# Kernel optimization log

Measured on AMD Instinct MI355X. Metric: run time of the kernel, lower is better.

## Reference

```python
import jax, jax.numpy as jnp
import numpy as np
from jax import lax

N_CLASS, SOS, EOS, NEG = 5, 0, 4, -10000.0


def _lstm_dir(x, Wih, Whh, bih, bhh, reverse):
    # x: (T, B, Din); PyTorch gate order i, f, g, o
    T, B, _ = x.shape
    Hd = Whh.shape[1]
    h0 = jnp.zeros((B, Hd), x.dtype)

    def step(carry, xt):
        h, c = carry
        g = xt @ Wih.T + h @ Whh.T + bih + bhh
        i, f, gg, o = jnp.split(g, 4, axis=-1)
        c = jax.nn.sigmoid(f) * c + jax.nn.sigmoid(i) * jnp.tanh(gg)
        h = jax.nn.sigmoid(o) * jnp.tanh(c)
        return (h, c), h

    xs = x[::-1] if reverse else x
    _, hs = lax.scan(step, (h0, h0), xs)
    return hs[::-1] if reverse else hs


def _forward(input_ids, tags, mask, emb, convs, lstm_params, lin_w, lin_b, transition):
    T, B = mask.shape
    x = emb[input_ids][:, None]  # (N, 1, L, E)
    pooled = []
    for w, b in convs:  # w: (K, 1, size, E)
        c = lax.conv_general_dilated(x, w, (1, 1), 'VALID',
                                     dimension_numbers=('NCHW', 'OIHW', 'NCHW'))
        c = jax.nn.relu(c[..., 0] + b[None, :, None])  # (N, K, L-size+1)
        pooled.append(jnp.max(c, axis=2))              # max-pool over length
    para = jnp.concatenate(pooled, axis=1)             # (N, 3K)
    h = para.reshape(B, T, -1).transpose(1, 0, 2)      # (T, B, 3K); equal para_len
    for (Wf, Uf, bf, cf, Wb, Ub, bb, cb) in lstm_params:  # 2-layer BiLSTM (eval: no dropout)
        hf = _lstm_dir(h, Wf, Uf, bf, cf, False)
        hb = _lstm_dir(h, Wb, Ub, bb, cb, True)
        h = jnp.concatenate([hf, hb], axis=-1)
    m = mask[..., None]
    feats = ((h * m) @ lin_w.T + lin_b) * m            # (T, B, 5)

    # CRF forward algorithm (log partition)
    alpha0 = jnp.full((B, N_CLASS), NEG, feats.dtype).at[:, SOS].set(0.0)

    def step(alpha, inp):
        feat, mt = inp
        s = alpha[:, None, :] + transition[None] + feat[:, :, None]
        new = jax.nn.logsumexp(s, axis=-1)
        return new * mt[:, None] + alpha * (1.0 - mt[:, None]), None

    alpha, _ = lax.scan(step, alpha0, (feats, mask))
    fwd_score = jax.nn.logsumexp(alpha + transition[EOS][None], axis=-1)

    # gold path score
    tags_ext = jnp.concatenate([jnp.full((1, B), SOS, tags.dtype), tags], 0)  # (T+1, B)
    emit = jnp.take_along_axis(feats, tags[..., None], axis=-1)[..., 0]       # (T, B)
    trans = transition[tags_ext[1:], tags_ext[:-1]]                           # (T, B)
    gold = jnp.sum((emit + trans) * mask, axis=0)
    lengths = mask.sum(0).astype(jnp.int32)
    last = tags_ext[lengths, jnp.arange(B)]
    gold = gold + transition[EOS, last]
    return (fwd_score - gold).sum()


def setup_inputs() -> dict:
    key = jax.random.key(0)
    ks = jax.random.split(key, 32)
    B, T, L, V, E, K, H = 8, 64, 64, 50000, 768, 256, 64
    N = B * T
    inp = {}
    inp['input_ids'] = jax.random.randint(ks[0], (N, L), 1, V)
    inp['tags'] = jax.random.randint(ks[1], (T, B), 1, 4)  # B/I/O tags
    inp['mask'] = jnp.ones((T, B), jnp.float32)
    inp['para_len'] = jnp.full((B,), T, jnp.int32)
    inp['emb'] = jax.random.normal(ks[2], (V, E)) * 0.1
    for i, sz in enumerate((3, 4, 5)):
        inp[f'cw{sz}'] = jax.random.normal(ks[3 + i], (K, 1, sz, E)) * (1.0 / np.sqrt(sz * E))
        inp[f'cb{sz}'] = jnp.zeros((K,), jnp.float32)
    kidx = 6
    for layer, din in ((0, 3 * K), (1, 2 * H)):
        for d in 'fb':
            inp[f'Wih{layer}{d}'] = jax.random.normal(ks[kidx], (4 * H, din)) * (1.0 / np.sqrt(din)); kidx += 1
            inp[f'Whh{layer}{d}'] = jax.random.normal(ks[kidx], (4 * H, H)) * (1.0 / np.sqrt(H)); kidx += 1
            inp[f'bih{layer}{d}'] = jnp.zeros((4 * H,), jnp.float32)
            inp[f'bhh{layer}{d}'] = jnp.zeros((4 * H,), jnp.float32)
    inp['lin_w'] = jax.random.normal(ks[kidx], (N_CLASS, 2 * H)) * 0.1; kidx += 1
    inp['lin_b'] = jnp.zeros((N_CLASS,), jnp.float32)
    tr = jax.random.normal(ks[kidx], (N_CLASS, N_CLASS))
    inp['transition'] = tr.at[SOS, :].set(NEG).at[:, EOS].set(NEG)
    return inp


def reference(input_ids, tags, mask, para_len, emb, cw3, cb3, cw4, cb4, cw5, cb5,
              Wih0f, Whh0f, bih0f, bhh0f, Wih0b, Whh0b, bih0b, bhh0b,
              Wih1f, Whh1f, bih1f, bhh1f, Wih1b, Whh1b, bih1b, bhh1b,
              lin_w, lin_b, transition):
    convs = ((cw3, cb3), (cw4, cb4), (cw5, cb5))
    lstm_params = ((Wih0f, Whh0f, bih0f, bhh0f, Wih0b, Whh0b, bih0b, bhh0b),
                   (Wih1f, Whh1f, bih1f, bhh1f, Wih1b, Whh1b, bih1b, bhh1b))
    return _forward(input_ids, tags, mask, emb, convs, lstm_params, lin_w, lin_b, transition)
```

## Files before the change

### kernel.cpp

```cpp
#include <hip/hip_runtime.h>
#include <cstdint>
#include <cstddef>

#define DEV __device__ __forceinline__

typedef __bf16 bf16x8 __attribute__((ext_vector_type(8)));
typedef float f32x4 __attribute__((ext_vector_type(4)));

#define NEG_VAL -10000.0f

DEV unsigned int f2bf(float f) {
    unsigned int u = __float_as_uint(f);
    return (u + 0x7FFFu + ((u >> 16) & 1u)) >> 16;
}
DEV unsigned int pk2(float a, float b) { return f2bf(a) | (f2bf(b) << 16); }

DEV float sigf(float x)  { return __builtin_amdgcn_rcpf(1.f + __expf(-x)); }
DEV float tanhff(float x){ return 2.f * __builtin_amdgcn_rcpf(1.f + __expf(-2.f * x)) - 1.f; }

__global__ void cast_all_kernel(const float* __restrict__ cw3,
                                const float* __restrict__ cw4,
                                const float* __restrict__ cw5,
                                const float* __restrict__ Wih0f,
                                const float* __restrict__ Wih0b,
                                const float* __restrict__ Wih1f,
                                const float* __restrict__ Wih1b,
                                unsigned short* __restrict__ wbc,
                                unsigned short* __restrict__ wih0c,
                                unsigned short* __restrict__ wih1c) {
    int tid = blockIdx.x * blockDim.x + threadIdx.x;
    const float* src;
    uint4* dstp;
    if (tid < 294912) {
        int g   = tid & 3;
        int col = (tid >> 2) & 255;
        int c   = (tid >> 10) % 24;
        int p   = tid / (24 * 256 * 4);
        int sz, j; const float* W;
        if (p < 3)      { sz = 3; j = p;     W = cw3; }
        else if (p < 7) { sz = 4; j = p - 3; W = cw4; }
        else            { sz = 5; j = p - 7; W = cw5; }
        src = W + ((size_t)col * sz + j) * 768 + c * 32 + g * 8;
        dstp = reinterpret_cast<uint4*>(wbc) +
               ((size_t)(p * 24 + c) * 1024 + (col >> 4) * 64 + g * 16 + (col & 15));
    } else if (tid < 294912 + 49152) {
        int u   = tid - 294912;
        int g   = u & 3;
        int col = (u >> 2) & 255;
        int kc  = (u >> 10) % 24;
        int dir = u / (24 * 256 * 4);
        const float* W = dir ? Wih0b : Wih0f;
        src = W + (size_t)col * 768 + kc * 32 + g * 8;
        dstp = reinterpret_cast<uint4*>(wih0c) +
               ((size_t)(dir * 24 + kc) * 1024 + (col >> 4) * 64 + g * 16 + (col & 15));
    } else if (tid < 294912 + 49152 + 8192) {
        int u   = tid - 294912 - 49152;
        int g   = u & 3;
        int col = (u >> 2) & 255;
        int kc  = (u >> 10) % 4;
        int dir = u / (4 * 256 * 4);
        const float* W = dir ? Wih1b : Wih1f;
        src = W + (size_t)col * 128 + kc * 32 + g * 8;
        dstp = reinterpret_cast<uint4*>(wih1c) +
               ((size_t)(dir * 4 + kc) * 1024 + (col >> 4) * 64 + g * 16 + (col & 15));
    } else return;
    float4 a = *(const float4*)(src);
    float4 b = *(const float4*)(src + 4);
    *dstp = make_uint4(pk2(a.x, a.y), pk2(a.z, a.w), pk2(b.x, b.y), pk2(b.z, b.w));
}

template<int SZ>
DEV void conv_body(const int* __restrict__ ids,
                   const float* __restrict__ emb,
                   const unsigned short* __restrict__ wbc,
                   const float* __restrict__ cb,
                   unsigned short* __restrict__ para_bf,
                   int pair, int szi, int pbase,
                   unsigned short* Xlds)
{
    int tid  = threadIdx.x;
    int lane = tid & 63;
    int nw   = tid >> 6;
    int l15  = lane & 15;
    int q    = lane >> 4;
    int n0   = pair * 2;

    int srow  = tid >> 1;
    int shalf = tid & 1;
    int sid   = ids[(n0 + (srow >> 6)) * 64 + (srow & 63)];
    const float* embrow = emb + (size_t)sid * 768 + shalf * 16;
    int skey = (srow >> 1) & 3;
    int xo0 = srow * 32 + (((2 * shalf)     ^ skey) * 8);
    int xo1 = srow * 32 + (((2 * shalf + 1) ^ skey) * 8);

    int vlaneB = nw * 2048 + lane * 8;

    f32x4 acc[8][4];
    #pragma unroll
    for (int a = 0; a < 8; a++)
        #pragma unroll
        for (int t = 0; t < 4; t++) acc[a][t] = (f32x4){0.f, 0.f, 0.f, 0.f};

    bf16x8 bfr[2][4];
    float4 e0, e1, e2, e3;

    {
        e0 = ((const float4*)embrow)[0];
        e1 = ((const float4*)embrow)[1];
        e2 = ((const float4*)embrow)[2];
        e3 = ((const float4*)embrow)[3];
        const unsigned short* bt = wbc + (size_t)(pbase * 24) * 8192 + vlaneB;
        #pragma unroll
        for (int t = 0; t < 4; t++)
            bfr[0][t] = *(const bf16x8*)(bt + t * 512);
        uint4 p0 = make_uint4(pk2(e0.x, e0.y), pk2(e0.z, e0.w),
                              pk2(e1.x, e1.y), pk2(e1.z, e1.w));
        uint4 p1 = make_uint4(pk2(e2.x, e2.y), pk2(e2.z, e2.w),
                              pk2(e3.x, e3.y), pk2(e3.z, e3.w));
        *(uint4*)&Xlds[xo0] = p0;
        *(uint4*)&Xlds[xo1] = p1;
        asm volatile("s_waitcnt lgkmcnt(0)" ::: "memory");
        __builtin_amdgcn_s_barrier();
    }

    int cbase = pbase * 24;
    for (int c2 = 0; c2 < 24; c2 += 2, cbase += 2) {
        #pragma unroll
        for (int s2 = 0; s2 < 2 * SZ; ++s2) {
            const int half = (s2 < SZ) ? 0 : 1;
            const int j    = s2 - half * SZ;
            const int par  = s2 & 1;
            {
                const int sP = s2 + 1;
                const int offP = (sP < SZ) ? sP * 24
                               : (sP < 2 * SZ ? (sP - SZ) * 24 + 1 : 2);
                const unsigned short* bt =
                    wbc + (size_t)(cbase + offP) * 8192 + vlaneB;
                #pragma unroll
                for (int t = 0; t < 4; t++)
                    bfr[par ^ 1][t] = *(const bf16x8*)(bt + t * 512);
            }
            if (s2 == 0 || s2 == SZ) {
                int cE = half ? c2 + 2 : c2 + 1; if (cE > 23) cE = 0;
                const float* sp = embrow + cE * 32;
                e0 = ((const float4*)sp)[0];
                e1 = ((const float4*)sp)[1];
                e2 = ((const float4*)sp)[2];
                e3 = ((const float4*)sp)[3];
            }

            const unsigned short* Xb = Xlds + half * 4096;
            {
                bf16x8 af[4];
                #pragma unroll
                for (int a = 0; a < 4; a++) {
                    int pp = 16 * a + l15 + j; if (pp > 63) pp = 63;
                    af[a] = *(const bf16x8*)(
                        &Xb[pp * 32 + ((q ^ ((pp >> 1) & 3)) * 8)]);
                }
                __builtin_amdgcn_s_setprio(1);
                #pragma unroll
                for (int a = 0; a < 4; a++)
                    #pragma unroll
                    for (int t = 0; t < 4; t++)
                        acc[a][t] = __builtin_amdgcn_mfma_f32_16x16x32_bf16(
                            af[a], bfr[par][t], acc[a][t], 0, 0, 0);
                __builtin_amdgcn_s_setprio(0);
            }
            {
                bf16x8 af[4];
                #pragma unroll
                for (int a = 0; a < 4; a++) {
                    int pp = 16 * a + l15 + j; if (pp > 63) pp = 63;
                    int xr = 64 + pp;
                    af[a] = *(const bf16x8*)(
                        &Xb[xr * 32 + ((q ^ ((xr >> 1) & 3)) * 8)]);
                }
                __builtin_amdgcn_s_setprio(1);
                #pragma unroll
                for (int a = 0; a < 4; a++)
                    #pragma unroll
                    for (int t = 0; t < 4; t++)
                        acc[4 + a][t] = __builtin_amdgcn_mfma_f32_16x16x32_bf16(
                            af[a], bfr[par][t], acc[4 + a][t], 0, 0, 0);
                __builtin_amdgcn_s_setprio(0);
            }

            if (j == SZ - 1) {
                unsigned short* Xw = Xlds + (half ^ 1) * 4096;
                uint4 p0 = make_uint4(pk2(e0.x, e0.y), pk2(e0.z, e0.w),
                                      pk2(e1.x, e1.y), pk2(e1.z, e1.w));
                uint4 p1 = make_uint4(pk2(e2.x, e2.y), pk2(e2.z, e2.w),
                                      pk2(e3.x, e3.y), pk2(e3.z, e3.w));
                *(uint4*)&Xw[xo0] = p0;
                *(uint4*)&Xw[xo1] = p1;
                asm volatile("s_waitcnt lgkmcnt(0)" ::: "memory");
                __builtin_amdgcn_s_barrier();
            }
        }
    }

    int pmax = 64 - SZ;
    #pragma unroll
    for (int t = 0; t < 4; t++) {
        int colb = nw * 64 + t * 16;
        float bias = cb[colb + l15];
        #pragma unroll
        for (int s = 0; s < 2; s++) {
            float m = 0.0f;
            #pragma unroll
            for (int a4 = 0; a4 < 4; a4++) {
                #pragma unroll
                for (int r = 0; r < 4; r++) {
                    int p = 16 * a4 + q * 4 + r;
                    float v = acc[s * 4 + a4][t][r] + bias;
                    v = v > 0.f ? v : 0.f;
                    if (p <= pmax) m = v > m ? v : m;
                }
            }
            m = fmaxf(m, __shfl_xor(m, 16));
            m = fmaxf(m, __shfl_xor(m, 32));
            if (lane < 16) {
                int n = n0 + s;
                int row = (n & 63) * 8 + (n >> 6);
                para_bf[(size_t)row * 768 + szi * 256 + colb + lane] =
                    (unsigned short)f2bf(m);
            }
        }
    }
}

__global__ __launch_bounds__(256, 2) void conv_pool_kernel(
    const int* __restrict__ ids,
    const float* __restrict__ emb,
    const unsigned short* __restrict__ wbc,
    const float* __restrict__ cb3, const float* __restrict__ cb4,
    const float* __restrict__ cb5,
    unsigned short* __restrict__ para_bf)
{
    __shared__ unsigned short Xlds[2][4096];
    int bx   = blockIdx.x;
    int szi  = 2 - (bx >> 8);
    int pair = bx & 255;
    if (szi == 0)
        conv_body<3>(ids, emb, wbc, cb3, para_bf, pair, 0, 0, &Xlds[0][0]);
    else if (szi == 1)
        conv_body<4>(ids, emb, wbc, cb4, para_bf, pair, 1, 3, &Xlds[0][0]);
    else
        conv_body<5>(ids, emb, wbc, cb5, para_bf, pair, 2, 7, &Xlds[0][0]);
}

template<int KC>
__global__ __launch_bounds__(256) void gemm_in_kernel(
    const unsigned short* __restrict__ xbf,
    const unsigned short* __restrict__ wihc,
    const float* __restrict__ bihF, const float* __restrict__ bhhF,
    const float* __restrict__ bihB, const float* __restrict__ bhhB,
    float* __restrict__ gates)
{
    const int din = KC * 32;
    int bx   = blockIdx.x;
    int dir  = bx >> 4;
    int rowg = (bx >> 1) & 7;
    int colg = bx & 1;
    int tid  = threadIdx.x;
    int lane = tid & 63;
    int wid  = tid >> 6;
    int mw   = wid >> 1;
    int nw   = wid & 1;
    int l15  = lane & 15;
    int q    = lane >> 4;

    const float* bih = dir ? bihB : bihF;
    const float* bhh = dir ? bhhB : bhhF;
    const unsigned short* wt = wihc + (size_t)dir * KC * 8192;

    const unsigned short* arow[2];
    #pragma unroll
    for (int a = 0; a < 2; a++)
        arow[a] = xbf + (size_t)(rowg * 64 + mw * 32 + a * 16 + l15) * din + q * 8;
    const unsigned short* bbase = wt + (colg * 8 + nw * 4) * 512 + lane * 8;

    f32x4 acc[2][4];
    #pragma unroll
    for (int a = 0; a < 2; a++)
        #pragma unroll
        for (int t = 0; t < 4; t++) acc[a][t] = (f32x4){0.f, 0.f, 0.f, 0.f};

    bf16x8 afb[3][2], bfb[3][4];
    #pragma unroll
    for (int s = 0; s < 3; s++) {
        int k0 = (s < KC) ? s : KC - 1;
        if (s < 2) {
            #pragma unroll
            for (int a = 0; a < 2; a++)
                afb[s][a] = *(const bf16x8*)(arow[a] + k0 * 32);
            #pragma unroll
            for (int t = 0; t < 4; t++)
                bfb[s][t] = *(const bf16x8*)(bbase + (size_t)k0 * 8192 + t * 512);
        }
    }

    #pragma unroll 3
    for (int kc = 0; kc < KC; ++kc) {
        const int p = kc % 3;
        int kn = (kc + 2 < KC) ? kc + 2 : KC - 1;
        const int pn = (kc + 2) % 3;
        #pragma unroll
        for (int a = 0; a < 2; a++)
            afb[pn][a] = *(const bf16x8*)(arow[a] + kn * 32);
        #pragma unroll
        for (int t = 0; t < 4; t++)
            bfb[pn][t] = *(const bf16x8*)(bbase + (size_t)kn * 8192 + t * 512);
        #pragma unroll
        for (int a = 0; a < 2; a++)
            #pragma unroll
            for (int t = 0; t < 4; t++)
                acc[a][t] = __builtin_amdgcn_mfma_f32_16x16x32_bf16(
                    afb[p][a], bfb[p][t], acc[a][t], 0, 0, 0);
    }

    #pragma unroll
    for (int t = 0; t < 4; t++) {
        int nn = colg * 128 + nw * 64 + t * 16 + l15;
        float bb = bih[nn] + bhh[nn];
        float* gp = gates + ((size_t)dir * 256 + nn) * 512 +
                    rowg * 64 + mw * 32 + q * 4;
        #pragma unroll
        for (int a = 0; a < 2; a++) {
            f32x4 v = acc[a][t];
            v[0] += bb; v[1] += bb; v[2] += bb; v[3] += bb;
            *(f32x4*)(gp + a * 16) = v;
        }
    }
}

__global__ __launch_bounds__(256) void lstm_rec_kernel(
    const float* __restrict__ gates,
    const float* __restrict__ WhhF, const float* __restrict__ WhhB,
    float* __restrict__ houtF,
    unsigned short* __restrict__ houtB)
{
    int dir = blockIdx.x;
    const float* Whh = dir ? WhhB : WhhF;
    const float* gin = gates + (size_t)dir * 256 * 512;

    __shared__ unsigned short h16[2][16 * 64];

    int tid  = threadIdx.x;
    int lane = tid & 63;
    int w    = tid >> 6;
    int l15  = lane & 15;
    int q    = lane >> 4;
    int hh   = 16 * w + l15;

    bf16x8 Bf[4][2];
    #pragma unroll
    for (int g = 0; g < 4; g++)
        #pragma unroll
        for (int kh = 0; kh < 2; kh++) {
            const float* wp = Whh + (size_t)(g * 64 + hh) * 64 + kh * 32 + q * 8;
            float4 f0 = *(const float4*)wp;
            float4 f1 = *(const float4*)(wp + 4);
            bf16x8 r;
            r[0] = (__bf16)f0.x; r[1] = (__bf16)f0.y;
            r[2] = (__bf16)f0.z; r[3] = (__bf16)f0.w;
            r[4] = (__bf16)f1.x; r[5] = (__bf16)f1.y;
            r[6] = (__bf16)f1.z; r[7] = (__bf16)f1.w;
            Bf[g][kh] = r;
        }

    const float* pg[4];
    #pragma unroll
    for (int g = 0; g < 4; g++)
        pg[g] = gin + ((size_t)(g * 64 + hh)) * 512 + 4 * q;

    for (int i = tid; i < 2 * 16 * 64; i += 256)
        ((unsigned short*)h16)[i] = 0;
    float cst[4] = {0.f, 0.f, 0.f, 0.f};
    __syncthreads();

    int t0 = dir ? 63 : 0;
    f32x4 gv[4];
    #pragma unroll
    for (int g = 0; g < 4; g++) gv[g] = *(const f32x4*)(pg[g] + t0 * 8);

    for (int s = 0; s < 64; ++s) {
        int t = dir ? 63 - s : s;
        const unsigned short* hb = h16[s & 1];
        int slot0 = q ^ (l15 & 7);
        int slot1 = (4 + q) ^ (l15 & 7);
        bf16x8 a0 = *(const bf16x8*)&hb[l15 * 64 + slot0 * 8];
        bf16x8 a1 = *(const bf16x8*)&hb[l15 * 64 + slot1 * 8];

        f32x4 acc[4];
        #pragma unroll
        for (int g = 0; g < 4; g++) {
            acc[g] = __builtin_amdgcn_mfma_f32_16x16x32_bf16(a0, Bf[g][0], gv[g], 0, 0, 0);
            acc[g] = __builtin_amdgcn_mfma_f32_16x16x32_bf16(a1, Bf[g][1], acc[g], 0, 0, 0);
        }

        int sn = (s + 1 < 64) ? s + 1 : 63;
        int t2 = dir ? 63 - sn : sn;
        f32x4 n0 = *(const f32x4*)(pg[0] + t2 * 8);
        f32x4 n1 = *(const f32x4*)(pg[1] + t2 * 8);
        f32x4 n2 = *(const f32x4*)(pg[2] + t2 * 8);
        f32x4 n3 = *(const f32x4*)(pg[3] + t2 * 8);

        if (q < 2) {
            unsigned short* hw = h16[(s + 1) & 1];
            #pragma unroll
            for (int r = 0; r < 4; r++) {
                int b = 4 * q + r;
                float gi = acc[0][r];
                float gf = acc[1][r];
                float gg = acc[2][r];
                float go = acc[3][r];
                float cn = sigf(gf) * cst[r] + sigf(gi) * tanhff(gg);
                float hv = sigf(go) * tanhff(cn);
                cst[r] = cn;
                int slot = (hh >> 3) ^ (b & 7);
                hw[b * 64 + slot * 8 + (hh & 7)] = (unsigned short)f2bf(hv);
                size_t oi = ((size_t)t * 8 + b) * 128 + dir * 64 + hh;
                if (houtF) houtF[oi] = hv;
                houtB[oi] = (unsigned short)f2bf(hv);
            }
        }
        __syncthreads();
        gv[0] = n0; gv[1] = n1; gv[2] = n2; gv[3] = n3;
    }
}

__global__ __launch_bounds__(512) void crf_kernel(
    const float* __restrict__ h1,
    const float* __restrict__ lin_w,
    const float* __restrict__ lin_b,
    const float* __restrict__ mask,
    const int* __restrict__ tags,
    const float* __restrict__ trans,
    float* __restrict__ out) {
    __shared__ float feats[64][8][5];
    __shared__ float wl[5][128];
    __shared__ float msk[512];
    __shared__ int   tgs[512];
    __shared__ float fwd_s[8], gold_s[8];
    __shared__ float tr[25], trE[5], lb[5];
    int tid = threadIdx.x;
    if (tid < 25) tr[tid] = trans[tid];
    if (tid < 5) { trE[tid] = trans[20 + tid]; lb[tid] = lin_b[tid]; }
    msk[tid] = mask[tid];
    tgs[tid] = tags[tid];
    if (tid < 128) {
        #pragma unroll
        for (int i = 0; i < 5; i++) wl[i][tid] = lin_w[i * 128 + tid];
    }
    __syncthreads();

    {
        const float4* h4 = (const float4*)(h1 + (size_t)tid * 128);
        float a0 = 0.f, a1 = 0.f, a2 = 0.f, a3 = 0.f, a4 = 0.f;
        for (int e4 = 0; e4 < 32; e4++) {
            float4 hv = h4[e4];
            int e = e4 * 4;
            a0 += hv.x * wl[0][e] + hv.y * wl[0][e+1] + hv.z * wl[0][e+2] + hv.w * wl[0][e+3];
            a1 += hv.x * wl[1][e] + hv.y * wl[1][e+1] + hv.z * wl[1][e+2] + hv.w * wl[1][e+3];
            a2 += hv.x * wl[2][e] + hv.y * wl[2][e+1] + hv.z * wl[2][e+2] + hv.w * wl[2][e+3];
            a3 += hv.x * wl[3][e] + hv.y * wl[3][e+1] + hv.z * wl[3][e+2] + hv.w * wl[3][e+3];
            a4 += hv.x * wl[4][e] + hv.y * wl[4][e+1] + hv.z * wl[4][e+2] + hv.w * wl[4][e+3];
        }
        float m = msk[tid];
        int t = tid >> 3, b = tid & 7;
        feats[t][b][0] = (m * a0 + lb[0]) * m;
        feats[t][b][1] = (m * a1 + lb[1]) * m;
        feats[t][b][2] = (m * a2 + lb[2]) * m;
        feats[t][b][3] = (m * a3 + lb[3]) * m;
        feats[t][b][4] = (m * a4 + lb[4]) * m;
    }
    __syncthreads();

    if (tid < 40) {
        int b = tid / 5, i = tid % 5;
        float alpha = (i == 0) ? 0.f : NEG_VAL;
        float trow[5];
        #pragma unroll
        for (int j2 = 0; j2 < 5; j2++) trow[j2] = tr[i * 5 + j2];
        for (int t = 0; t < 64; t++) {
            float s0, s1, s2, s3, s4;
            s0 = __shfl(alpha, b * 5 + 0, 64) + trow[0];
            s1 = __shfl(alpha, b * 5 + 1, 64) + trow[1];
            s2 = __shfl(alpha, b * 5 + 2, 64) + trow[2];
            s3 = __shfl(alpha, b * 5 + 3, 64) + trow[3];
            s4 = __shfl(alpha, b * 5 + 4, 64) + trow[4];
            float mx = fmaxf(fmaxf(fmaxf(s0, s1), fmaxf(s2, s3)), s4);
            float sum = expf(s0 - mx) + expf(s1 - mx) + expf(s2 - mx) +
                        expf(s3 - mx) + expf(s4 - mx);
            float lse = mx + logf(sum) + feats[t][b][i];
            float mt = msk[t * 8 + b];
            alpha = mt * lse + (1.f - mt) * alpha;
        }
        float v = alpha + trE[i];
        float m0 = __shfl(v, b * 5 + 0, 64);
        float m1 = __shfl(v, b * 5 + 1, 64);
        float m2 = __shfl(v, b * 5 + 2, 64);
        float m3 = __shfl(v, b * 5 + 3, 64);
        float m4 = __shfl(v, b * 5 + 4, 64);
        float mx = fmaxf(fmaxf(fmaxf(m0, m1), fmaxf(m2, m3)), m4);
        float sum = expf(m0 - mx) + expf(m1 - mx) + expf(m2 - mx) +
                    expf(m3 - mx) + expf(m4 - mx);
        if (i == 0) fwd_s[b] = mx + logf(sum);
    }
    if (tid >= 64 && tid < 72) {
        int b = tid - 64;
        float g = 0.f, lenf = 0.f;
        int prev = 0;
        for (int t = 0; t < 64; t++) {
            int tg = tgs[t * 8 + b];
            float mt = msk[t * 8 + b];
            g += (feats[t][b][tg] + tr[tg * 5 + prev]) * mt;
            lenf += mt;
            prev = tg;
        }
        int len = (int)lenf;
        int last = (len == 0) ? 0 : tgs[(len - 1) * 8 + b];
        g += trE[last];
        gold_s[b] = g;
    }
    __syncthreads();
    if (tid == 0) {
        float s = 0.f;
        for (int b = 0; b < 8; b++) s += fwd_s[b] - gold_s[b];
        out[0] = s;
    }
}

extern "C" void kernel_launch(void* const* d_in, const int* in_sizes, int n_in,
                              void* d_out, int out_size, void* d_ws, size_t ws_size,
                              hipStream_t stream) {
    const int*   ids   = (const int*)d_in[0];
    const int*   tags  = (const int*)d_in[1];
    const float* mask  = (const float*)d_in[2];
    const float* emb   = (const float*)d_in[4];
    const float* cw3   = (const float*)d_in[5];
    const float* cb3   = (const float*)d_in[6];
    const float* cw4   = (const float*)d_in[7];
    const float* cb4   = (const float*)d_in[8];
    const float* cw5   = (const float*)d_in[9];
    const float* cb5   = (const float*)d_in[10];
    const float* Wih0f = (const float*)d_in[11];
    const float* Whh0f = (const float*)d_in[12];
    const float* bih0f = (const float*)d_in[13];
    const float* bhh0f = (const float*)d_in[14];
    const float* Wih0b = (const float*)d_in[15];
    const float* Whh0b = (const float*)d_in[16];
    const float* bih0b = (const float*)d_in[17];
    const float* bhh0b = (const float*)d_in[18];
    const float* Wih1f = (const float*)d_in[19];
    const float* Whh1f = (const float*)d_in[20];
    const float* bih1f = (const float*)d_in[21];
    const float* bhh1f = (const float*)d_in[22];
    const float* Wih1b = (const float*)d_in[23];
    const float* Whh1b = (const float*)d_in[24];
    const float* bih1b = (const float*)d_in[25];
    const float* bhh1b = (const float*)d_in[26];
    const float* lin_w = (const float*)d_in[27];
    const float* lin_b = (const float*)d_in[28];
    const float* trans = (const float*)d_in[29];

    char* ws = (char*)d_ws;
    unsigned short* wbc     = (unsigned short*)ws;
    unsigned short* wih0c   = (unsigned short*)(ws + 4718592);
    unsigned short* wih1c   = (unsigned short*)(ws + 5505024);
    unsigned short* para_bf = (unsigned short*)(ws + 5636096);
    float*          gates   = (float*)(ws + 6422528);
    unsigned short* h0_bf   = (unsigned short*)(ws + 5636096);
    float*          h1f     = (float*)(ws + 4718592);

    hipLaunchKernelGGL(cast_all_kernel, dim3(1376), dim3(256), 0, stream,
                       cw3, cw4, cw5, Wih0f, Wih0b, Wih1f, Wih1b,
                       wbc, wih0c, wih1c);
    hipLaunchKernelGGL(conv_pool_kernel, dim3(768), dim3(256), 0, stream,
                       ids, emb, wbc, cb3, cb4, cb5, para_bf);
    hipLaunchKernelGGL((gemm_in_kernel<24>), dim3(32), dim3(256), 0, stream,
                       para_bf, wih0c, bih0f, bhh0f, bih0b, bhh0b, gates);
    hipLaunchKernelGGL(lstm_rec_kernel, dim3(2), dim3(256), 0, stream,
                       gates, Whh0f, Whh0b, (float*)nullptr, h0_bf);
    hipLaunchKernelGGL((gemm_in_kernel<4>), dim3(32), dim3(256), 0, stream,
                       h0_bf, wih1c, bih1f, bhh1f, bih1b, bhh1b, gates);
    hipLaunchKernelGGL(lstm_rec_kernel, dim3(2), dim3(256), 0, stream,
                       gates, Whh1f, Whh1b, h1f, h0_bf);
    hipLaunchKernelGGL(crf_kernel, dim3(1), dim3(512), 0, stream,
                       h1f, lin_w, lin_b, mask, tags, trans, (float*)d_out);
}
```

Before: 275.3 us.

## Deepen gate prefetch in LSTM recurrence and reorder gates layout time-major

The input-projection GEMM now writes its gate pre-activations in a time-major layout, so each recurrence step reads one contiguous 8 KB slice instead of strided rows. The recurrence kernel prefetches gate inputs three steps ahead through a 4-slot register ring instead of one step ahead, hiding global load latency on the serial critical path. The GEMM's operand prefetch also grows from depth 2 to depth 3. The extra buffers raise register pressure, and the GEMM's output stores become more scattered.

```diff
diff --git a/kernel.cpp b/kernel.cpp
--- a/kernel.cpp
+++ b/kernel.cpp
@@ -256,7 +256,7 @@
     const unsigned short* __restrict__ wihc,
     const float* __restrict__ bihF, const float* __restrict__ bhhF,
     const float* __restrict__ bihB, const float* __restrict__ bhhB,
-    float* __restrict__ gates)
+    float* __restrict__ gates2)
 {
     const int din = KC * 32;
     int bx   = blockIdx.x;
@@ -287,25 +287,23 @@
         #pragma unroll
         for (int t = 0; t < 4; t++) acc[a][t] = (f32x4){0.f, 0.f, 0.f, 0.f};
 
-    bf16x8 afb[3][2], bfb[3][4];
+    bf16x8 afb[4][2], bfb[4][4];
     #pragma unroll
     for (int s = 0; s < 3; s++) {
         int k0 = (s < KC) ? s : KC - 1;
-        if (s < 2) {
-            #pragma unroll
-            for (int a = 0; a < 2; a++)
-                afb[s][a] = *(const bf16x8*)(arow[a] + k0 * 32);
-            #pragma unroll
-            for (int t = 0; t < 4; t++)
-                bfb[s][t] = *(const bf16x8*)(bbase + (size_t)k0 * 8192 + t * 512);
-        }
-    }
-
-    #pragma unroll 3
+        #pragma unroll
+        for (int a = 0; a < 2; a++)
+            afb[s][a] = *(const bf16x8*)(arow[a] + k0 * 32);
+        #pragma unroll
+        for (int t = 0; t < 4; t++)
+            bfb[s][t] = *(const bf16x8*)(bbase + (size_t)k0 * 8192 + t * 512);
+    }
+
+    #pragma unroll 4
     for (int kc = 0; kc < KC; ++kc) {
-        const int p = kc % 3;
-        int kn = (kc + 2 < KC) ? kc + 2 : KC - 1;
-        const int pn = (kc + 2) % 3;
+        const int p  = kc & 3;
+        const int pn = (kc + 3) & 3;
+        int kn = (kc + 3 < KC) ? kc + 3 : KC - 1;
         #pragma unroll
         for (int a = 0; a < 2; a++)
             afb[pn][a] = *(const bf16x8*)(arow[a] + kn * 32);
@@ -321,29 +319,29 @@
     }
 
     #pragma unroll
-    for (int t = 0; t < 4; t++) {
-        int nn = colg * 128 + nw * 64 + t * 16 + l15;
+    for (int tt = 0; tt < 4; tt++) {
+        int nn = colg * 128 + nw * 64 + tt * 16 + l15;
         float bb = bih[nn] + bhh[nn];
-        float* gp = gates + ((size_t)dir * 256 + nn) * 512 +
-                    rowg * 64 + mw * 32 + q * 4;
         #pragma unroll
         for (int a = 0; a < 2; a++) {
-            f32x4 v = acc[a][t];
+            int m = rowg * 64 + mw * 32 + q * 4 + a * 16;
+            int tcol = m >> 3, b0 = m & 7;
+            f32x4 v = acc[a][tt];
             v[0] += bb; v[1] += bb; v[2] += bb; v[3] += bb;
-            *(f32x4*)(gp + a * 16) = v;
+            *(f32x4*)(gates2 + (((size_t)dir * 64 + tcol) * 256 + nn) * 8 + b0) = v;
         }
     }
 }
 
 __global__ __launch_bounds__(256) void lstm_rec_kernel(
-    const float* __restrict__ gates,
+    const float* __restrict__ gates2,
     const float* __restrict__ WhhF, const float* __restrict__ WhhB,
     float* __restrict__ houtF,
     unsigned short* __restrict__ houtB)
 {
     int dir = blockIdx.x;
     const float* Whh = dir ? WhhB : WhhF;
-    const float* gin = gates + (size_t)dir * 256 * 512;
+    const float* gin = gates2 + (size_t)dir * 64 * 256 * 8;
 
     __shared__ unsigned short h16[2][16 * 64];
 
@@ -370,22 +368,28 @@
             Bf[g][kh] = r;
         }
 
-    const float* pg[4];
+    const float* pgB[4];
     #pragma unroll
     for (int g = 0; g < 4; g++)
-        pg[g] = gin + ((size_t)(g * 64 + hh)) * 512 + 4 * q;
+        pgB[g] = gin + (size_t)(g * 64 + hh) * 8 + 4 * q;
 
     for (int i = tid; i < 2 * 16 * 64; i += 256)
         ((unsigned short*)h16)[i] = 0;
     float cst[4] = {0.f, 0.f, 0.f, 0.f};
     __syncthreads();
 
-    int t0 = dir ? 63 : 0;
-    f32x4 gv[4];
-    #pragma unroll
-    for (int g = 0; g < 4; g++) gv[g] = *(const f32x4*)(pg[g] + t0 * 8);
-
+    f32x4 gvp[4][4];
+    #pragma unroll
+    for (int d = 0; d < 3; d++) {
+        int td = dir ? 63 - d : d;
+        #pragma unroll
+        for (int g = 0; g < 4; g++)
+            gvp[d][g] = *(const f32x4*)(pgB[g] + (size_t)td * 2048);
+    }
+
+    #pragma unroll 4
     for (int s = 0; s < 64; ++s) {
+        const int slot = s & 3;
         int t = dir ? 63 - s : s;
         const unsigned short* hb = h16[s & 1];
         int slot0 = q ^ (l15 & 7);
@@ -396,16 +400,18 @@
         f32x4 acc[4];
         #pragma unroll
         for (int g = 0; g < 4; g++) {
-            acc[g] = __builtin_amdgcn_mfma_f32_16x16x32_bf16(a0, Bf[g][0], gv[g], 0, 0, 0);
+            acc[g] = __builtin_amdgcn_mfma_f32_16x16x32_bf16(a0, Bf[g][0], gvp[slot][g], 0, 0, 0);
             acc[g] = __builtin_amdgcn_mfma_f32_16x16x32_bf16(a1, Bf[g][1], acc[g], 0, 0, 0);
         }
 
-        int sn = (s + 1 < 64) ? s + 1 : 63;
-        int t2 = dir ? 63 - sn : sn;
-        f32x4 n0 = *(const f32x4*)(pg[0] + t2 * 8);
-        f32x4 n1 = *(const f32x4*)(pg[1] + t2 * 8);
-        f32x4 n2 = *(const f32x4*)(pg[2] + t2 * 8);
-        f32x4 n3 = *(const f32x4*)(pg[3] + t2 * 8);
+        {
+            int sn = (s + 3 < 64) ? s + 3 : 63;
+            int tn = dir ? 63 - sn : sn;
+            const int slotn = (s + 3) & 3;
+            #pragma unroll
+            for (int g = 0; g < 4; g++)
+                gvp[slotn][g] = *(const f32x4*)(pgB[g] + (size_t)tn * 2048);
+        }
 
         if (q < 2) {
             unsigned short* hw = h16[(s + 1) & 1];
@@ -419,15 +425,14 @@
                 float cn = sigf(gf) * cst[r] + sigf(gi) * tanhff(gg);
                 float hv = sigf(go) * tanhff(cn);
                 cst[r] = cn;
-                int slot = (hh >> 3) ^ (b & 7);
-                hw[b * 64 + slot * 8 + (hh & 7)] = (unsigned short)f2bf(hv);
+                int slotw = (hh >> 3) ^ (b & 7);
+                hw[b * 64 + slotw * 8 + (hh & 7)] = (unsigned short)f2bf(hv);
                 size_t oi = ((size_t)t * 8 + b) * 128 + dir * 64 + hh;
                 if (houtF) houtF[oi] = hv;
                 houtB[oi] = (unsigned short)f2bf(hv);
             }
         }
         __syncthreads();
-        gv[0] = n0; gv[1] = n1; gv[2] = n2; gv[3] = n3;
     }
 }
 
```

After: 250.3 us, median of 3. 1.1x faster.
